# Performance work log

Measured on AMD Instinct MI355X. Metric: run time of the kernel, lower is better.

## Reference

```python
import jax, jax.numpy as jnp
import numpy as np

A = 128       # atom_fea_len
NBR = 41      # nbr_fea_len
H = 128       # h_fea_len_dist == h_fea_len_const
NCONV = 3
EPS = 1e-5    # BatchNorm eps


def leaky(x):
    return jnp.where(x >= 0, x, 0.01 * x)  # LeakyReLU(0.01)


def bn(x2d, g, b):
    # training-mode BatchNorm1d: batch statistics over dim 0 (biased variance)
    mu = x2d.mean(0)
    var = x2d.var(0)
    return g * (x2d - mu) * jax.lax.rsqrt(var + EPS) + b


def setup_inputs() -> dict:
    N, M = 20000, 12
    key = jax.random.key(0)
    ks = jax.random.split(key, 24)
    s = 0.02
    in2 = 2 * A + NBR  # 297
    d = {}
    d["atom_fea"] = jax.random.normal(ks[0], (N, 92), jnp.float32)
    d["nbr_fea"] = jax.random.uniform(ks[1], (N, M, NBR), dtype=jnp.float32)
    d["nbr_fea_offset"] = jax.random.normal(ks[2], (N, M, 3), jnp.float32)
    d["atom_pos"] = jax.random.normal(ks[3], (N, 3), jnp.float32) * 3.0
    d["cells"] = jnp.eye(3, dtype=jnp.float32) * 10.0 + 0.1 * jax.random.normal(ks[4], (3, 3), jnp.float32)
    d["nbr_fea_idx"] = jax.random.randint(ks[5], (N, M), 0, N)
    # embedding
    d["emb_W"] = s * jax.random.normal(ks[6], (A, 92), jnp.float32)
    d["emb_b"] = jnp.zeros((A,), jnp.float32)
    # conv layers (stacked)
    d["convs_W"] = s * jax.random.normal(ks[7], (NCONV, 2 * A, in2), jnp.float32)
    d["convs_b"] = jnp.zeros((NCONV, 2 * A), jnp.float32)
    d["convs_bn1_g"] = jnp.ones((NCONV, 2 * A), jnp.float32)
    d["convs_bn1_b"] = jnp.zeros((NCONV, 2 * A), jnp.float32)
    d["convs_bn2_g"] = jnp.ones((NCONV, A), jnp.float32)
    d["convs_bn2_b"] = jnp.zeros((NCONV, A), jnp.float32)
    # bond_distance head
    d["dist_W"] = s * jax.random.normal(ks[8], (H, in2), jnp.float32)
    d["dist_b"] = jnp.zeros((H,), jnp.float32)
    d["dist_bn_g"] = jnp.ones((H,), jnp.float32)
    d["dist_bn_b"] = jnp.zeros((H,), jnp.float32)
    d["dist2_W"] = s * jax.random.normal(ks[9], (1, H), jnp.float32)
    d["dist2_b"] = jnp.zeros((1,), jnp.float32)
    # bond_constant head
    d["const_W"] = s * jax.random.normal(ks[10], (H, in2), jnp.float32)
    d["const_b"] = jnp.zeros((H,), jnp.float32)
    d["const_bn_g"] = jnp.ones((H,), jnp.float32)
    d["const_bn_b"] = jnp.zeros((H,), jnp.float32)
    d["const2_W"] = s * jax.random.normal(ks[11], (1, H), jnp.float32)
    d["const2_b"] = jnp.zeros((1,), jnp.float32)
    return d


def _forward(atom_fea, nbr_fea, nbr_fea_offset, atom_pos, cells,
             emb_W, emb_b, convs_W, convs_b, convs_bn1_g, convs_bn1_b,
             convs_bn2_g, convs_bn2_b, dist_W, dist_b, dist_bn_g, dist_bn_b,
             dist2_W, dist2_b, const_W, const_b, const_bn_g, const_bn_b,
             const2_W, const2_b, nbr_fea_idx):
    N, M = nbr_fea_idx.shape
    af = atom_fea @ emb_W.T + emb_b  # (N, A) embedding

    # get_distance: PBC distance using fractional offsets and the cell matrix
    nbr_abs = atom_pos[nbr_fea_idx] + jnp.einsum('nmk,kd->nmd', nbr_fea_offset, cells)
    dvec = nbr_abs - atom_pos[:, None, :]
    distance = jnp.sqrt(jnp.sum(dvec * dvec, -1, keepdims=True) + 1e-12)  # (N, M, 1)

    # conv layers: gather -> concat -> linear -> bn -> gate -> sum -> bn -> residual
    for i in range(NCONV):
        total = jnp.concatenate([
            jnp.broadcast_to(af[:, None, :], (N, M, A)),
            af[nbr_fea_idx],
            nbr_fea], axis=2)                                   # (N, M, 2A+NBR)
        g = jnp.einsum('nmf,of->nmo', total, convs_W[i]) + convs_b[i]  # (N, M, 2A)
        g = bn(g.reshape(-1, 2 * A), convs_bn1_g[i], convs_bn1_b[i]).reshape(N, M, 2 * A)
        nbr_filter = jax.nn.sigmoid(g[..., :A])
        nbr_core = leaky(g[..., A:])
        summed = bn((nbr_filter * nbr_core).sum(1), convs_bn2_g[i], convs_bn2_b[i])
        af = leaky(af + summed)

    # bond features
    bond_fea = jnp.concatenate([
        jnp.broadcast_to(af[:, None, :], (N, M, A)),
        af[nbr_fea_idx],
        nbr_fea], axis=2)  # (N, M, 2A+NBR)

    # bond_distance head (LeakyReLU activations)
    bd = jnp.einsum('nmf,hf->nmh', bond_fea, dist_W) + dist_b
    bd = leaky(bn(bd.reshape(-1, H), dist_bn_g, dist_bn_b).reshape(N, M, H))
    bd = leaky(jnp.einsum('nmh,oh->nmo', bd, dist2_W) + dist2_b + distance)  # (N, M, 1)

    # bond_constant head (Softplus activations)
    bc = jnp.einsum('nmf,hf->nmh', bond_fea, const_W) + const_b
    bc = jax.nn.softplus(bn(bc.reshape(-1, H), const_bn_g, const_bn_b).reshape(N, M, H))
    bc = jax.nn.softplus(jnp.einsum('nmh,oh->nmo', bc, const2_W) + const2_b)  # (N, M, 1)

    return jnp.concatenate([bd, bc], axis=-1)  # (N, M, 2)


def reference(atom_fea, nbr_fea, nbr_fea_offset, atom_pos, cells,
              emb_W, emb_b, convs_W, convs_b, convs_bn1_g, convs_bn1_b,
              convs_bn2_g, convs_bn2_b, dist_W, dist_b, dist_bn_g, dist_bn_b,
              dist2_W, dist2_b, const_W, const_b, const_bn_g, const_bn_b,
              const2_W, const2_b, nbr_fea_idx):
    return _forward(atom_fea, nbr_fea, nbr_fea_offset, atom_pos, cells,
                    emb_W, emb_b, convs_W, convs_b, convs_bn1_g, convs_bn1_b,
                    convs_bn2_g, convs_bn2_b, dist_W, dist_b, dist_bn_g, dist_bn_b,
                    dist2_W, dist2_b, const_W, const_b, const_bn_g, const_bn_b,
                    const2_W, const2_b, nbr_fea_idx)
```

## Files before the change

kernel.cpp:

```cpp
#include <hip/hip_runtime.h>
#include <hip/hip_bf16.h>
#include <math.h>

typedef __hip_bfloat16 bf16;

#define AFEA 128
#define NBRF 41
#define IN2 297
#define KP 320
#define TSTR 328
#define ROWS 64
#define P1 64
#define P2 16

typedef __attribute__((ext_vector_type(8))) short bf16x8;
typedef __attribute__((ext_vector_type(4))) float f32x4;

__device__ __forceinline__ unsigned short bfbits(float x) {
    bf16 h = __float2bfloat16(x);
    return *(unsigned short*)&h;
}
__device__ __forceinline__ unsigned int pack2(float x, float y) {
    return (unsigned int)bfbits(x) | ((unsigned int)bfbits(y) << 16);
}
__device__ __forceinline__ float blo(unsigned int u) { return __uint_as_float(u << 16); }
__device__ __forceinline__ float bhi(unsigned int u) { return __uint_as_float(u & 0xffff0000u); }
__device__ __forceinline__ float leakyf(float x) { return x >= 0.f ? x : 0.01f * x; }
__device__ __forceinline__ float sigmoid_fast(float x) { return 1.f / (1.f + __expf(-x)); }
__device__ __forceinline__ float softplus_fast(float x) {
    return fmaxf(x, 0.f) + __logf(1.f + __expf(-fabsf(x)));
}

__global__ void nbr16_kernel(const float* __restrict__ nbr, unsigned short* __restrict__ nbr16,
                             int NM)
{
    int i = blockIdx.x * blockDim.x + threadIdx.x;
    if (i >= NM * 64) return;
    int k = i & 63, e = i >> 6;
    nbr16[i] = (k < NBRF) ? bfbits(nbr[(size_t)e * NBRF + k]) : 0;
}

__global__ __launch_bounds__(256) void embed_kernel(
    const float* __restrict__ xf, const float* __restrict__ W,
    const float* __restrict__ b, float* __restrict__ af,
    unsigned short* __restrict__ af16, int N)
{
    __shared__ float W_s[92 * 128];
    __shared__ float xs[16 * 92];
    int t = threadIdx.x;
    int n0 = blockIdx.x * 16;
    for (int i = t; i < 92 * 128; i += 256) {
        int o = i / 92, k = i - o * 92;
        W_s[k * 128 + o] = W[i];
    }
    for (int i = t; i < 16 * 92; i += 256) {
        int a = i / 92, k = i - a * 92;
        int n = n0 + a;
        xs[i] = (n < N) ? xf[(size_t)n * 92 + k] : 0.f;
    }
    __syncthreads();
    int o = t & 127, h = t >> 7;
    float bias = b[o];
    for (int a = h; a < 16; a += 2) {
        int n = n0 + a;
        if (n >= N) break;
        float acc = bias;
        const float* xr = xs + a * 92;
        #pragma unroll 4
        for (int k = 0; k < 92; k++) acc += xr[k] * W_s[k * 128 + o];
        af[(size_t)n * AFEA + o] = acc;
        af16[(size_t)n * AFEA + o] = bfbits(acc);
    }
}

__global__ void prep_kernel(const float* __restrict__ Wa, size_t offA,
                            const float* __restrict__ Wsrc, size_t offB,
                            unsigned short* __restrict__ Wb,
                            float* __restrict__ zbuf, int nz)
{
    int i = blockIdx.x * blockDim.x + threadIdx.x;
    if (i < nz) zbuf[i] = 0.f;
    if (i >= KP * 256) return;
    int t32 = i & 31;
    int c = (i >> 5) & 255;
    int kc = i >> 13;
    int k = kc * 32 + t32;
    float v = 0.f;
    if (k < IN2) v = (c < 128) ? Wa[offA + (size_t)c * IN2 + k]
                               : Wsrc[offB + (size_t)(c - 128) * IN2 + k];
    Wb[i] = bfbits(v);
}

__global__ __launch_bounds__(256, 3) void gemm_mfma_kernel(
    const unsigned short* __restrict__ af16, const unsigned short* __restrict__ nbr16,
    const int* __restrict__ idx, const unsigned short* __restrict__ Wb,
    const float* __restrict__ bias_a, size_t boffA,
    const float* __restrict__ bias_b, size_t boffB,
    unsigned short* __restrict__ g_t, float* __restrict__ part1,
    int NM, int M)
{
    __shared__ unsigned short a_tile[ROWS * TSTR];
    const int t = threadIdx.x;
    const int e0 = blockIdx.x * ROWS;

    const int l = t & 63, w = t >> 6;
    const int m16 = l & 15, q = l >> 4;
    const int colbase = w * 64;
    const unsigned short* bbase = Wb + (size_t)(colbase + m16) * 32 + q * 8;

    {
        int row = t >> 2, p = t & 3;
        int e = e0 + row;
        int n = e / M;
        int j = idx[e];
        const uint4* srcn = (const uint4*)(af16 + (size_t)n * AFEA);
        const uint4* srcj = (const uint4*)(af16 + (size_t)j * AFEA);
        const uint4* srcb = (const uint4*)(nbr16 + (size_t)e * 64);
        uint4* dst = (uint4*)(a_tile + row * TSTR);
        #pragma unroll
        for (int u = 0; u < 4; u++) dst[p + 4 * u] = srcn[p + 4 * u];
        #pragma unroll
        for (int u = 0; u < 4; u++) dst[16 + p + 4 * u] = srcj[p + 4 * u];
        #pragma unroll
        for (int u = 0; u < 2; u++) dst[32 + p + 4 * u] = srcb[p + 4 * u];
    }

    bf16x8 bcur[4], bnxt[4];
    #pragma unroll
    for (int ct = 0; ct < 4; ct++)
        bcur[ct] = *(const bf16x8*)(bbase + ct * 512);
    #pragma unroll
    for (int ct = 0; ct < 4; ct++)
        bnxt[ct] = *(const bf16x8*)(bbase + 8192 + ct * 512);

    __syncthreads();

    f32x4 acc[4][4];
    #pragma unroll
    for (int rt = 0; rt < 4; rt++)
        #pragma unroll
        for (int ct = 0; ct < 4; ct++) acc[rt][ct] = (f32x4)0.f;

    const unsigned short* abase = a_tile + m16 * TSTR + q * 8;

    #pragma unroll
    for (int kc = 0; kc < KP / 32; kc++) {
        bf16x8 a[4], b2[4];
        if (kc < KP / 32 - 2) {
            #pragma unroll
            for (int ct = 0; ct < 4; ct++)
                b2[ct] = *(const bf16x8*)(bbase + (kc + 2) * 8192 + ct * 512);
        }
        #pragma unroll
        for (int rt = 0; rt < 4; rt++)
            a[rt] = *(const bf16x8*)(abase + rt * 16 * TSTR + kc * 32);
        #pragma unroll
        for (int rt = 0; rt < 4; rt++)
            #pragma unroll
            for (int ct = 0; ct < 4; ct++)
                acc[rt][ct] = __builtin_amdgcn_mfma_f32_16x16x32_bf16(
                    a[rt], bcur[ct], acc[rt][ct], 0, 0, 0);
        if (kc < KP / 32 - 1) {
            #pragma unroll
            for (int ct = 0; ct < 4; ct++) bcur[ct] = bnxt[ct];
        }
        if (kc < KP / 32 - 2) {
            #pragma unroll
            for (int ct = 0; ct < 4; ct++) bnxt[ct] = b2[ct];
        }
    }

    float* pp = part1 + (size_t)(blockIdx.x & (P1 - 1)) * 512;
    #pragma unroll
    for (int ct = 0; ct < 4; ct++) {
        int col = colbase + ct * 16 + m16;
        float bias = (col < 128) ? bias_a[boffA + col] : bias_b[boffB + col - 128];
        float ps = 0.f, pq = 0.f;
        #pragma unroll
        for (int rt = 0; rt < 4; rt++) {
            float v0 = acc[rt][ct][0] + bias;
            float v1 = acc[rt][ct][1] + bias;
            float v2 = acc[rt][ct][2] + bias;
            float v3 = acc[rt][ct][3] + bias;
            ps += (v0 + v1) + (v2 + v3);
            pq += (v0 * v0 + v1 * v1) + (v2 * v2 + v3 * v3);
            uint2 pk;
            pk.x = pack2(v0, v1);
            pk.y = pack2(v2, v3);
            *(uint2*)(g_t + (size_t)col * NM + e0 + rt * 16 + q * 4) = pk;
        }
        ps += __shfl_xor(ps, 16); ps += __shfl_xor(ps, 32);
        pq += __shfl_xor(pq, 16); pq += __shfl_xor(pq, 32);
        if (q == 0) {
            atomicAdd(&pp[col], ps);
            atomicAdd(&pp[256 + col], pq);
        }
    }
}

__global__ __launch_bounds__(256) void gate_kernel(
    const unsigned short* __restrict__ gt, const float* __restrict__ part1,
    const float* __restrict__ gamma, const float* __restrict__ beta,
    float* __restrict__ summed, float* __restrict__ part2,
    float cnt1, int N, int M, int NM)
{
    __shared__ float affA[4 * 16], affC[4 * 16];
    int t = threadIdx.x, w = t >> 6, l = t & 63;
    int cp0 = (blockIdx.x & 3) * 16 + w * 4;
    int fch0 = 2 * cp0;

    if (l < 16) {
        int ch = (l < 8) ? (fch0 + l) : (128 + fch0 + (l - 8));
        float s = 0.f, qq = 0.f;
        #pragma unroll 8
        for (int p = 0; p < P1; p++) {
            s += part1[(size_t)p * 512 + ch];
            qq += part1[(size_t)p * 512 + 256 + ch];
        }
        float mean = s / cnt1;
        float var = fmaxf(qq / cnt1 - mean * mean, 0.f);
        float a = gamma[ch] * rsqrtf(var + 1e-5f);
        affA[w * 16 + l] = a;
        affC[w * 16 + l] = beta[ch] - mean * a;
    }
    __syncthreads();

    int n = (blockIdx.x >> 2) * 64 + l;
    bool act = (n < N);
    size_t col0 = (size_t)n * M;
    float* pp = part2 + (size_t)(blockIdx.x & (P2 - 1)) * 256;
    #pragma unroll
    for (int cpi = 0; cpi < 4; cpi++) {
        int chf = fch0 + 2 * cpi;
        int chc = 128 + chf;
        float s0 = 0.f, s1 = 0.f;
        if (act) {
            const uint2* rf0 = (const uint2*)(gt + (size_t)chf * NM + col0);
            const uint2* rf1 = (const uint2*)(gt + (size_t)(chf + 1) * NM + col0);
            const uint2* rc0 = (const uint2*)(gt + (size_t)chc * NM + col0);
            const uint2* rc1 = (const uint2*)(gt + (size_t)(chc + 1) * NM + col0);
            float aF0 = affA[w * 16 + 2 * cpi],     cF0 = affC[w * 16 + 2 * cpi];
            float aF1 = affA[w * 16 + 2 * cpi + 1], cF1 = affC[w * 16 + 2 * cpi + 1];
            float aC0 = affA[w * 16 + 8 + 2 * cpi],     cC0 = affC[w * 16 + 8 + 2 * cpi];
            float aC1 = affA[w * 16 + 8 + 2 * cpi + 1], cC1 = affC[w * 16 + 8 + 2 * cpi + 1];
            #pragma unroll
            for (int u = 0; u < 3; u++) {
                uint2 f0 = rf0[u], f1 = rf1[u], k0 = rc0[u], k1 = rc1[u];
                #pragma unroll
                for (int h = 0; h < 4; h++) {
                    unsigned int fw0 = (h < 2) ? f0.x : f0.y;
                    unsigned int fw1 = (h < 2) ? f1.x : f1.y;
                    unsigned int kw0 = (h < 2) ? k0.x : k0.y;
                    unsigned int kw1 = (h < 2) ? k1.x : k1.y;
                    float gf0 = (h & 1) ? bhi(fw0) : blo(fw0);
                    float gf1 = (h & 1) ? bhi(fw1) : blo(fw1);
                    float gc0 = (h & 1) ? bhi(kw0) : blo(kw0);
                    float gc1 = (h & 1) ? bhi(kw1) : blo(kw1);
                    s0 += sigmoid_fast(fmaf(aF0, gf0, cF0)) * leakyf(fmaf(aC0, gc0, cC0));
                    s1 += sigmoid_fast(fmaf(aF1, gf1, cF1)) * leakyf(fmaf(aC1, gc1, cC1));
                }
            }
            *(float2*)(summed + (size_t)n * AFEA + chf) = make_float2(s0, s1);
        }
        float q0 = s0 * s0, q1 = s1 * s1;
        #pragma unroll
        for (int sft = 32; sft > 0; sft >>= 1) {
            s0 += __shfl_xor(s0, sft);
            s1 += __shfl_xor(s1, sft);
            q0 += __shfl_xor(q0, sft);
            q1 += __shfl_xor(q1, sft);
        }
        if (l == 0) {
            atomicAdd(&pp[chf], s0);
            atomicAdd(&pp[chf + 1], s1);
            atomicAdd(&pp[128 + chf], q0);
            atomicAdd(&pp[128 + chf + 1], q1);
        }
    }
}

__global__ __launch_bounds__(256) void afup_kernel(
    float* __restrict__ af, unsigned short* __restrict__ af16,
    const float* __restrict__ summed, const float* __restrict__ part2,
    const float* __restrict__ gamma2, const float* __restrict__ beta2,
    float cnt2, int total)
{
    __shared__ float a2s[128], c2s[128];
    int t = threadIdx.x;
    if (t < 128) {
        float s = 0.f, qq = 0.f;
        #pragma unroll
        for (int p = 0; p < P2; p++) {
            s += part2[(size_t)p * 256 + t];
            qq += part2[(size_t)p * 256 + 128 + t];
        }
        float mean = s / cnt2;
        float var = fmaxf(qq / cnt2 - mean * mean, 0.f);
        float a = gamma2[t] * rsqrtf(var + 1e-5f);
        a2s[t] = a;
        c2s[t] = beta2[t] - mean * a;
    }
    __syncthreads();
    int o = t & 127;
    float a2 = a2s[o], c2 = c2s[o];
    int base = blockIdx.x * 2048 + t;
    #pragma unroll
    for (int k = 0; k < 8; k++) {
        int i = base + k * 256;
        if (i < total) {
            float v = af[i] + a2 * summed[i] + c2;
            v = (v >= 0.f) ? v : 0.01f * v;
            af[i] = v;
            af16[i] = bfbits(v);
        }
    }
}

__global__ __launch_bounds__(256) void head_kernel(
    const unsigned short* __restrict__ gt, const float* __restrict__ part1,
    const float* __restrict__ dbg, const float* __restrict__ cbg,
    const float* __restrict__ dbb, const float* __restrict__ cbb,
    const float* __restrict__ w2d, const float* __restrict__ b2d,
    const float* __restrict__ w2c, const float* __restrict__ b2c,
    const float* __restrict__ pos, const float* __restrict__ off,
    const float* __restrict__ cells, const int* __restrict__ idx,
    float* __restrict__ out, float cnt1, int NM, int M)
{
    __shared__ float a_s[256], c_s[256], w_s[256];
    int t = threadIdx.x;
    {
        float s = 0.f, qq = 0.f;
        #pragma unroll 8
        for (int p = 0; p < P1; p++) {
            s += part1[(size_t)p * 512 + t];
            qq += part1[(size_t)p * 512 + 256 + t];
        }
        float mean = s / cnt1;
        float var = fmaxf(qq / cnt1 - mean * mean, 0.f);
        float g  = (t < 128) ? dbg[t] : cbg[t - 128];
        float be = (t < 128) ? dbb[t] : cbb[t - 128];
        float a = g * rsqrtf(var + 1e-5f);
        a_s[t] = a;
        c_s[t] = be - mean * a;
        w_s[t] = (t < 128) ? w2d[t] : w2c[t - 128];
    }
    __syncthreads();

    int e = blockIdx.x * 512 + t * 2;
    if (e >= NM) return;
    float sd0 = 0.f, sd1 = 0.f, sc0 = 0.f, sc1 = 0.f;
    #pragma unroll 4
    for (int ch = 0; ch < 128; ch++) {
        unsigned int u = *(const unsigned int*)(gt + (size_t)ch * NM + e);
        float a = a_s[ch], c = c_s[ch], wv = w_s[ch];
        sd0 += leakyf(fmaf(a, blo(u), c)) * wv;
        sd1 += leakyf(fmaf(a, bhi(u), c)) * wv;
    }
    #pragma unroll 4
    for (int ch = 128; ch < 256; ch++) {
        unsigned int u = *(const unsigned int*)(gt + (size_t)ch * NM + e);
        float a = a_s[ch], c = c_s[ch], wv = w_s[ch];
        sc0 += softplus_fast(fmaf(a, blo(u), c)) * wv;
        sc1 += softplus_fast(fmaf(a, bhi(u), c)) * wv;
    }
    float dist[2];
    #pragma unroll
    for (int h = 0; h < 2; h++) {
        int eb = e + h;
        int n = eb / M;
        int j = idx[eb];
        float o0 = off[(size_t)eb * 3 + 0];
        float o1 = off[(size_t)eb * 3 + 1];
        float o2 = off[(size_t)eb * 3 + 2];
        float d0 = o0 * cells[0] + o1 * cells[3] + o2 * cells[6] + pos[(size_t)j * 3 + 0] - pos[(size_t)n * 3 + 0];
        float d1 = o0 * cells[1] + o1 * cells[4] + o2 * cells[7] + pos[(size_t)j * 3 + 1] - pos[(size_t)n * 3 + 1];
        float d2 = o0 * cells[2] + o1 * cells[5] + o2 * cells[8] + pos[(size_t)j * 3 + 2] - pos[(size_t)n * 3 + 2];
        dist[h] = sqrtf(d0 * d0 + d1 * d1 + d2 * d2 + 1e-12f);
    }
    float bd = b2d[0], bc = b2c[0];
    float4 o4;
    o4.x = leakyf(sd0 + bd + dist[0]);
    o4.y = softplus_fast(sc0 + bc);
    o4.z = leakyf(sd1 + bd + dist[1]);
    o4.w = softplus_fast(sc1 + bc);
    *(float4*)(out + (size_t)e * 2) = o4;
}

extern "C" void kernel_launch(void* const* d_in, const int* in_sizes, int n_in,
                              void* d_out, int out_size, void* d_ws, size_t ws_size,
                              hipStream_t stream) {
    const float* atom_fea   = (const float*)d_in[0];
    const float* nbr_fea    = (const float*)d_in[1];
    const float* nbr_off    = (const float*)d_in[2];
    const float* atom_pos   = (const float*)d_in[3];
    const float* cells      = (const float*)d_in[4];
    const int*   idx        = (const int*)d_in[5];
    const float* emb_W      = (const float*)d_in[6];
    const float* emb_b      = (const float*)d_in[7];
    const float* convs_W    = (const float*)d_in[8];
    const float* convs_b    = (const float*)d_in[9];
    const float* bn1g       = (const float*)d_in[10];
    const float* bn1b       = (const float*)d_in[11];
    const float* bn2g       = (const float*)d_in[12];
    const float* bn2b       = (const float*)d_in[13];
    const float* dist_W     = (const float*)d_in[14];
    const float* dist_b     = (const float*)d_in[15];
    const float* dist_bn_g  = (const float*)d_in[16];
    const float* dist_bn_b  = (const float*)d_in[17];
    const float* dist2_W    = (const float*)d_in[18];
    const float* dist2_b    = (const float*)d_in[19];
    const float* const_W    = (const float*)d_in[20];
    const float* const_b    = (const float*)d_in[21];
    const float* const_bn_g = (const float*)d_in[22];
    const float* const_bn_b = (const float*)d_in[23];
    const float* const2_W   = (const float*)d_in[24];
    const float* const2_b   = (const float*)d_in[25];

    const int N  = in_sizes[0] / 92;
    const int M  = in_sizes[5] / N;
    const int NM = N * M;

    char* ws = (char*)d_ws;
    size_t off = 0;
    float* af             = (float*)(ws + off); off += (size_t)N * AFEA * 4;
    float* summed         = (float*)(ws + off); off += (size_t)N * AFEA * 4;
    unsigned short* af16  = (unsigned short*)(ws + off); off += (size_t)N * AFEA * 2;
    unsigned short* Wb    = (unsigned short*)(ws + off); off += (size_t)256 * KP * 2;
    float* part1          = (float*)(ws + off); off += (size_t)P1 * 512 * 4;
    float* part2          = (float*)(ws + off); off += (size_t)P2 * 256 * 4;
    unsigned short* g_t   = (unsigned short*)(ws + off); off += (size_t)NM * 256 * 2;
    unsigned short* nbr16 = (unsigned short*)(ws + off); off += (size_t)NM * 64 * 2;

    const int NPART = P1 * 512 + P2 * 256;

    nbr16_kernel<<<(NM * 64 + 255) / 256, 256, 0, stream>>>(nbr_fea, nbr16, NM);
    embed_kernel<<<(N + 15) / 16, 256, 0, stream>>>(atom_fea, emb_W, emb_b, af, af16, N);

    const int gblocks = NM / ROWS;
    const int gateblocks = ((N + 63) / 64) * 4;
    const int prepblocks = (256 * KP + 255) / 256;

    for (int i = 0; i < 3; i++) {
        size_t wo  = (size_t)i * 256 * IN2;
        size_t bo  = (size_t)i * 256;
        size_t b2o = (size_t)i * 128;

        prep_kernel<<<prepblocks, 256, 0, stream>>>(
            convs_W, wo, convs_W, wo + (size_t)128 * IN2, Wb, part1, NPART);
        gemm_mfma_kernel<<<gblocks, 256, 0, stream>>>(
            af16, nbr16, idx, Wb, convs_b, bo, convs_b, bo + 128,
            g_t, part1, NM, M);
        gate_kernel<<<gateblocks, 256, 0, stream>>>(
            g_t, part1, bn1g + bo, bn1b + bo, summed, part2, (float)NM, N, M, NM);
        afup_kernel<<<(N * AFEA + 2047) / 2048, 256, 0, stream>>>(
            af, af16, summed, part2, bn2g + b2o, bn2b + b2o, (float)N, N * AFEA);
    }

    {
        prep_kernel<<<prepblocks, 256, 0, stream>>>(
            dist_W, 0, const_W, 0, Wb, part1, P1 * 512);
        gemm_mfma_kernel<<<gblocks, 256, 0, stream>>>(
            af16, nbr16, idx, Wb, dist_b, 0, const_b, 0,
            g_t, part1, NM, M);
        head_kernel<<<(NM + 511) / 512, 256, 0, stream>>>(
            g_t, part1, dist_bn_g, const_bn_g, dist_bn_b, const_bn_b,
            dist2_W, dist2_b, const2_W, const2_b,
            atom_pos, nbr_off, cells, idx, (float*)d_out, (float)NM, NM, M);
    }
}
```

Baseline: 675.5 us.

## Make gather-GEMM persistent with double-buffered async global-to-LDS loads

The gather GEMM becomes a persistent kernel with a grid of at most 512 blocks, each looping over 64-row tiles. The next tile's gathered rows (atom, neighbour atom, bond features) are prefetched into a second LDS buffer with global_load_lds direct-to-LDS loads while the current tile is computed. The LDS layout changes to a k-chunk-major arrangement, and weights are kept in a 4-deep register ring. This is meant to hide gather latency and launch overhead, at the cost of doubled LDS use, lower occupancy (launch bounds go from 3 to 2 blocks per unit), and reliance on the async LDS loads being ordered by the barrier.

```diff
diff --git a/kernel.cpp b/kernel.cpp
--- a/kernel.cpp
+++ b/kernel.cpp
@@ -8,8 +8,8 @@
 #define NBRF 41
 #define IN2 297
 #define KP 320
-#define TSTR 328
 #define ROWS 64
+#define GBLK 512
 #define P1 64
 #define P2 16
 
@@ -29,6 +29,14 @@
 __device__ __forceinline__ float sigmoid_fast(float x) { return 1.f / (1.f + __expf(-x)); }
 __device__ __forceinline__ float softplus_fast(float x) {
     return fmaxf(x, 0.f) + __logf(1.f + __expf(-fabsf(x)));
+}
+
+__device__ __forceinline__ void gload16(const unsigned short* g, unsigned short* lds) {
+    auto g1 = (const __attribute__((address_space(1))) void*)(
+        reinterpret_cast<uintptr_t>(g));
+    auto l3 = (__attribute__((address_space(3))) void*)(
+        (unsigned int)(reinterpret_cast<uintptr_t>(lds)));
+    __builtin_amdgcn_global_load_lds(g1, l3, 16, 0, 0);
 }
 
 __global__ void nbr16_kernel(const float* __restrict__ nbr, unsigned short* __restrict__ nbr16,
@@ -91,110 +99,136 @@
     Wb[i] = bfbits(v);
 }
 
-__global__ __launch_bounds__(256, 3) void gemm_mfma_kernel(
+__global__ __launch_bounds__(256, 2) void gemm_mfma_kernel(
     const unsigned short* __restrict__ af16, const unsigned short* __restrict__ nbr16,
     const int* __restrict__ idx, const unsigned short* __restrict__ Wb,
     const float* __restrict__ bias_a, size_t boffA,
     const float* __restrict__ bias_b, size_t boffB,
     unsigned short* __restrict__ g_t, float* __restrict__ part1,
-    int NM, int M)
-{
-    __shared__ unsigned short a_tile[ROWS * TSTR];
+    int NM, int M, int ntiles)
+{
+    __shared__ unsigned short a_tile[2][40 * 512];
+
     const int t = threadIdx.x;
-    const int e0 = blockIdx.x * ROWS;
-
     const int l = t & 63, w = t >> 6;
     const int m16 = l & 15, q = l >> 4;
     const int colbase = w * 64;
     const unsigned short* bbase = Wb + (size_t)(colbase + m16) * 32 + q * 8;
 
-    {
-        int row = t >> 2, p = t & 3;
-        int e = e0 + row;
-        int n = e / M;
-        int j = idx[e];
-        const uint4* srcn = (const uint4*)(af16 + (size_t)n * AFEA);
-        const uint4* srcj = (const uint4*)(af16 + (size_t)j * AFEA);
-        const uint4* srcb = (const uint4*)(nbr16 + (size_t)e * 64);
-        uint4* dst = (uint4*)(a_tile + row * TSTR);
-        #pragma unroll
-        for (int u = 0; u < 4; u++) dst[p + 4 * u] = srcn[p + 4 * u];
-        #pragma unroll
-        for (int u = 0; u < 4; u++) dst[16 + p + 4 * u] = srcj[p + 4 * u];
-        #pragma unroll
-        for (int u = 0; u < 2; u++) dst[32 + p + 4 * u] = srcb[p + 4 * u];
-    }
-
-    bf16x8 bcur[4], bnxt[4];
+    int tile = blockIdx.x;
+
+    bf16x8 bb[4][4];
     #pragma unroll
-    for (int ct = 0; ct < 4; ct++)
-        bcur[ct] = *(const bf16x8*)(bbase + ct * 512);
-    #pragma unroll
-    for (int ct = 0; ct < 4; ct++)
-        bnxt[ct] = *(const bf16x8*)(bbase + 8192 + ct * 512);
-
+    for (int c = 0; c < 4; c++)
+        #pragma unroll
+        for (int ct = 0; ct < 4; ct++)
+            bb[c][ct] = *(const bf16x8*)(bbase + c * 8192 + ct * 512);
+
+    int jreg = 0;
+    if (tile < ntiles) {
+        int e = tile * ROWS + l;
+        int j0 = idx[e];
+        int n0 = e / M;
+        unsigned short* bp = a_tile[0];
+        const unsigned short* srcn = af16 + (size_t)n0 * AFEA;
+        const unsigned short* srcj = af16 + (size_t)j0 * AFEA;
+        const unsigned short* srcb = nbr16 + (size_t)e * 64;
+        #pragma unroll
+        for (int i = 0; i < 4; i++) gload16(srcn + (4 * w + i) * 8, bp + (4 * w + i) * 512);
+        #pragma unroll
+        for (int i = 0; i < 4; i++) gload16(srcj + (4 * w + i) * 8, bp + (16 + 4 * w + i) * 512);
+        #pragma unroll
+        for (int i = 0; i < 2; i++) gload16(srcb + (2 * w + i) * 8, bp + (32 + 2 * w + i) * 512);
+        int e1 = (tile + GBLK) * ROWS + l;
+        jreg = idx[e1 < NM ? e1 : 0];
+    }
     __syncthreads();
 
-    f32x4 acc[4][4];
-    #pragma unroll
-    for (int rt = 0; rt < 4; rt++)
-        #pragma unroll
-        for (int ct = 0; ct < 4; ct++) acc[rt][ct] = (f32x4)0.f;
-
-    const unsigned short* abase = a_tile + m16 * TSTR + q * 8;
-
-    #pragma unroll
-    for (int kc = 0; kc < KP / 32; kc++) {
-        bf16x8 a[4], b2[4];
-        if (kc < KP / 32 - 2) {
-            #pragma unroll
-            for (int ct = 0; ct < 4; ct++)
-                b2[ct] = *(const bf16x8*)(bbase + (kc + 2) * 8192 + ct * 512);
-        }
+    int it = 0;
+    for (; tile < ntiles; tile += GBLK, it ^= 1) {
+        const int e0 = tile * ROWS;
+        unsigned short* bufc = a_tile[it];
+        unsigned short* bufn = a_tile[it ^ 1];
+
+        if (tile + GBLK < ntiles) {
+            int en = (tile + GBLK) * ROWS + l;
+            int nn = en / M;
+            const unsigned short* srcn = af16 + (size_t)nn * AFEA;
+            const unsigned short* srcj = af16 + (size_t)jreg * AFEA;
+            const unsigned short* srcb = nbr16 + (size_t)en * 64;
+            #pragma unroll
+            for (int i = 0; i < 4; i++) gload16(srcn + (4 * w + i) * 8, bufn + (4 * w + i) * 512);
+            #pragma unroll
+            for (int i = 0; i < 4; i++) gload16(srcj + (4 * w + i) * 8, bufn + (16 + 4 * w + i) * 512);
+            #pragma unroll
+            for (int i = 0; i < 2; i++) gload16(srcb + (2 * w + i) * 8, bufn + (32 + 2 * w + i) * 512);
+            int e2 = en + GBLK * ROWS;
+            jreg = idx[e2 < NM ? e2 : 0];
+        }
+
+        f32x4 acc[4][4];
         #pragma unroll
         for (int rt = 0; rt < 4; rt++)
-            a[rt] = *(const bf16x8*)(abase + rt * 16 * TSTR + kc * 32);
-        #pragma unroll
-        for (int rt = 0; rt < 4; rt++)
-            #pragma unroll
-            for (int ct = 0; ct < 4; ct++)
-                acc[rt][ct] = __builtin_amdgcn_mfma_f32_16x16x32_bf16(
-                    a[rt], bcur[ct], acc[rt][ct], 0, 0, 0);
-        if (kc < KP / 32 - 1) {
-            #pragma unroll
-            for (int ct = 0; ct < 4; ct++) bcur[ct] = bnxt[ct];
-        }
-        if (kc < KP / 32 - 2) {
-            #pragma unroll
-            for (int ct = 0; ct < 4; ct++) bnxt[ct] = b2[ct];
-        }
-    }
-
-    float* pp = part1 + (size_t)(blockIdx.x & (P1 - 1)) * 512;
-    #pragma unroll
-    for (int ct = 0; ct < 4; ct++) {
-        int col = colbase + ct * 16 + m16;
-        float bias = (col < 128) ? bias_a[boffA + col] : bias_b[boffB + col - 128];
-        float ps = 0.f, pq = 0.f;
-        #pragma unroll
-        for (int rt = 0; rt < 4; rt++) {
-            float v0 = acc[rt][ct][0] + bias;
-            float v1 = acc[rt][ct][1] + bias;
-            float v2 = acc[rt][ct][2] + bias;
-            float v3 = acc[rt][ct][3] + bias;
-            ps += (v0 + v1) + (v2 + v3);
-            pq += (v0 * v0 + v1 * v1) + (v2 * v2 + v3 * v3);
-            uint2 pk;
-            pk.x = pack2(v0, v1);
-            pk.y = pack2(v2, v3);
-            *(uint2*)(g_t + (size_t)col * NM + e0 + rt * 16 + q * 4) = pk;
-        }
-        ps += __shfl_xor(ps, 16); ps += __shfl_xor(ps, 32);
-        pq += __shfl_xor(pq, 16); pq += __shfl_xor(pq, 32);
-        if (q == 0) {
-            atomicAdd(&pp[col], ps);
-            atomicAdd(&pp[256 + col], pq);
-        }
+            #pragma unroll
+            for (int ct = 0; ct < 4; ct++) acc[rt][ct] = (f32x4)0.f;
+
+        const unsigned short* abase = bufc + q * 512 + m16 * 8;
+
+        #pragma unroll
+        for (int kc = 0; kc < KP / 32; kc++) {
+            bf16x8 a[4];
+            #pragma unroll
+            for (int rt = 0; rt < 4; rt++)
+                a[rt] = *(const bf16x8*)(abase + kc * 2048 + rt * 128);
+            #pragma unroll
+            for (int rt = 0; rt < 4; rt++)
+                #pragma unroll
+                for (int ct = 0; ct < 4; ct++)
+                    acc[rt][ct] = __builtin_amdgcn_mfma_f32_16x16x32_bf16(
+                        a[rt], bb[kc & 3][ct], acc[rt][ct], 0, 0, 0);
+            if (kc < 6) {
+                #pragma unroll
+                for (int ct = 0; ct < 4; ct++)
+                    bb[kc & 3][ct] = *(const bf16x8*)(bbase + (kc + 4) * 8192 + ct * 512);
+            }
+        }
+
+        if (tile + GBLK < ntiles) {
+            #pragma unroll
+            for (int c = 0; c < 4; c++)
+                #pragma unroll
+                for (int ct = 0; ct < 4; ct++)
+                    bb[c][ct] = *(const bf16x8*)(bbase + c * 8192 + ct * 512);
+        }
+
+        float* pp = part1 + (size_t)(blockIdx.x & (P1 - 1)) * 512;
+        #pragma unroll
+        for (int ct = 0; ct < 4; ct++) {
+            int col = colbase + ct * 16 + m16;
+            float bias = (col < 128) ? bias_a[boffA + col] : bias_b[boffB + col - 128];
+            float ps = 0.f, pq = 0.f;
+            #pragma unroll
+            for (int rt = 0; rt < 4; rt++) {
+                float v0 = acc[rt][ct][0] + bias;
+                float v1 = acc[rt][ct][1] + bias;
+                float v2 = acc[rt][ct][2] + bias;
+                float v3 = acc[rt][ct][3] + bias;
+                ps += (v0 + v1) + (v2 + v3);
+                pq += (v0 * v0 + v1 * v1) + (v2 * v2 + v3 * v3);
+                uint2 pk;
+                pk.x = pack2(v0, v1);
+                pk.y = pack2(v2, v3);
+                *(uint2*)(g_t + (size_t)col * NM + e0 + rt * 16 + q * 4) = pk;
+            }
+            ps += __shfl_xor(ps, 16); ps += __shfl_xor(ps, 32);
+            pq += __shfl_xor(pq, 16); pq += __shfl_xor(pq, 32);
+            if (q == 0) {
+                atomicAdd(&pp[col], ps);
+                atomicAdd(&pp[256 + col], pq);
+            }
+        }
+
+        __syncthreads();
     }
 }
 
@@ -437,6 +471,7 @@
     embed_kernel<<<(N + 15) / 16, 256, 0, stream>>>(atom_fea, emb_W, emb_b, af, af16, N);
 
     const int gblocks = NM / ROWS;
+    const int ggrid = gblocks < GBLK ? gblocks : GBLK;
     const int gateblocks = ((N + 63) / 64) * 4;
     const int prepblocks = (256 * KP + 255) / 256;
 
@@ -447,9 +482,9 @@
 
         prep_kernel<<<prepblocks, 256, 0, stream>>>(
             convs_W, wo, convs_W, wo + (size_t)128 * IN2, Wb, part1, NPART);
-        gemm_mfma_kernel<<<gblocks, 256, 0, stream>>>(
+        gemm_mfma_kernel<<<ggrid, 256, 0, stream>>>(
             af16, nbr16, idx, Wb, convs_b, bo, convs_b, bo + 128,
-            g_t, part1, NM, M);
+            g_t, part1, NM, M, gblocks);
         gate_kernel<<<gateblocks, 256, 0, stream>>>(
             g_t, part1, bn1g + bo, bn1b + bo, summed, part2, (float)NM, N, M, NM);
         afup_kernel<<<(N * AFEA + 2047) / 2048, 256, 0, stream>>>(
@@ -459,9 +494,9 @@
     {
         prep_kernel<<<prepblocks, 256, 0, stream>>>(
             dist_W, 0, const_W, 0, Wb, part1, P1 * 512);
-        gemm_mfma_kernel<<<gblocks, 256, 0, stream>>>(
+        gemm_mfma_kernel<<<ggrid, 256, 0, stream>>>(
             af16, nbr16, idx, Wb, dist_b, 0, const_b, 0,
-            g_t, part1, NM, M);
+            g_t, part1, NM, M, gblocks);
         head_kernel<<<(NM + 511) / 512, 256, 0, stream>>>(
             g_t, part1, dist_bn_g, const_bn_g, dist_bn_b, const_bn_b,
             dist2_W, dist2_b, const2_W, const2_b,
```

New measurement: 806.9 us. +19.5%, slower.

## Recompute conv GEMM in two passes instead of storing gated activations

Applied to the files above, without the earlier changes.

Each conv layer now runs the gather-GEMM twice. The first pass only accumulates BatchNorm statistics. The second recomputes the GEMM and applies BN, sigmoid·leaky gating and the neighbour sum in the epilogue through LDS, with atomics into the summed buffer. This removes the write and reread of the large channel-major g_t intermediate, at the cost of doubling MFMA and gather work. Weight preparation for all four GEMMs is also hoisted into one kernel, using a channel permutation so filter and core channels land in the same wave. A separate sumstats kernel and bn1fin kernel are added, and zeroing moves into other kernels.

```diff
diff --git a/kernel.cpp b/kernel.cpp
--- a/kernel.cpp
+++ b/kernel.cpp
@@ -12,6 +12,7 @@
 #define ROWS 64
 #define P1 64
 #define P2 16
+#define LSP 130
 
 typedef __attribute__((ext_vector_type(8))) short bf16x8;
 typedef __attribute__((ext_vector_type(4))) float f32x4;
@@ -29,6 +30,12 @@
 __device__ __forceinline__ float sigmoid_fast(float x) { return 1.f / (1.f + __expf(-x)); }
 __device__ __forceinline__ float softplus_fast(float x) {
     return fmaxf(x, 0.f) + __logf(1.f + __expf(-fabsf(x)));
+}
+
+__device__ __forceinline__ int permch(int slot) {
+    int w = slot >> 6, ct = (slot >> 4) & 3, m = slot & 15;
+    int base = w * 32 + (ct & 1) * 16 + m;
+    return (ct < 2) ? base : 128 + base;
 }
 
 __global__ void nbr16_kernel(const float* __restrict__ nbr, unsigned short* __restrict__ nbr16,
@@ -73,40 +80,38 @@
     }
 }
 
-__global__ void prep_kernel(const float* __restrict__ Wa, size_t offA,
-                            const float* __restrict__ Wsrc, size_t offB,
-                            unsigned short* __restrict__ Wb,
-                            float* __restrict__ zbuf, int nz)
+__global__ void prep_all_kernel(const float* __restrict__ convs_W,
+                                const float* __restrict__ dist_W,
+                                const float* __restrict__ const_W,
+                                unsigned short* __restrict__ Wb4,
+                                float* __restrict__ zbuf, int nz)
 {
     int i = blockIdx.x * blockDim.x + threadIdx.x;
     if (i < nz) zbuf[i] = 0.f;
-    if (i >= KP * 256) return;
-    int t32 = i & 31;
-    int c = (i >> 5) & 255;
-    int kc = i >> 13;
+    if (i >= 4 * KP * 256) return;
+    int s = i / (KP * 256);
+    int r = i - s * (KP * 256);
+    int t32 = r & 31;
+    int c = (r >> 5) & 255;
+    int kc = r >> 13;
     int k = kc * 32 + t32;
     float v = 0.f;
-    if (k < IN2) v = (c < 128) ? Wa[offA + (size_t)c * IN2 + k]
-                               : Wsrc[offB + (size_t)(c - 128) * IN2 + k];
-    Wb[i] = bfbits(v);
-}
-
-__global__ __launch_bounds__(256, 3) void gemm_mfma_kernel(
+    if (k < IN2) {
+        if (s < 3) v = convs_W[((size_t)s * 256 + permch(c)) * IN2 + k];
+        else       v = (c < 128) ? dist_W[(size_t)c * IN2 + k]
+                                 : const_W[(size_t)(c - 128) * IN2 + k];
+    }
+    Wb4[i] = bfbits(v);
+}
+
+__device__ __forceinline__ void gemm_core(
     const unsigned short* __restrict__ af16, const unsigned short* __restrict__ nbr16,
     const int* __restrict__ idx, const unsigned short* __restrict__ Wb,
-    const float* __restrict__ bias_a, size_t boffA,
-    const float* __restrict__ bias_b, size_t boffB,
-    unsigned short* __restrict__ g_t, float* __restrict__ part1,
-    int NM, int M)
-{
-    __shared__ unsigned short a_tile[ROWS * TSTR];
-    const int t = threadIdx.x;
-    const int e0 = blockIdx.x * ROWS;
-
+    unsigned short* a_tile, int e0, int M, int t, f32x4 (&acc)[4][4])
+{
     const int l = t & 63, w = t >> 6;
     const int m16 = l & 15, q = l >> 4;
-    const int colbase = w * 64;
-    const unsigned short* bbase = Wb + (size_t)(colbase + m16) * 32 + q * 8;
+    const unsigned short* bbase = Wb + (size_t)(w * 64 + m16) * 32 + q * 8;
 
     {
         int row = t >> 2, p = t & 3;
@@ -135,7 +140,6 @@
 
     __syncthreads();
 
-    f32x4 acc[4][4];
     #pragma unroll
     for (int rt = 0; rt < 4; rt++)
         #pragma unroll
@@ -169,12 +173,197 @@
             for (int ct = 0; ct < 4; ct++) bnxt[ct] = b2[ct];
         }
     }
-
+}
+
+__global__ __launch_bounds__(256, 3) void gemm_stats_kernel(
+    const unsigned short* __restrict__ af16, const unsigned short* __restrict__ nbr16,
+    const int* __restrict__ idx, const unsigned short* __restrict__ Wb,
+    const float* __restrict__ bias256, float* __restrict__ part1,
+    float* __restrict__ summed, int NM, int M, int nsum)
+{
+    __shared__ __align__(16) unsigned short a_tile[ROWS * TSTR];
+    int t = threadIdx.x;
+    for (int i = blockIdx.x * 256 + t; i < nsum; i += gridDim.x * 256) summed[i] = 0.f;
+
+    f32x4 acc[4][4];
+    gemm_core(af16, nbr16, idx, Wb, a_tile, blockIdx.x * ROWS, M, t, acc);
+
+    const int l = t & 63, w = t >> 6, m16 = l & 15, q = l >> 4;
     float* pp = part1 + (size_t)(blockIdx.x & (P1 - 1)) * 512;
     #pragma unroll
     for (int ct = 0; ct < 4; ct++) {
-        int col = colbase + ct * 16 + m16;
-        float bias = (col < 128) ? bias_a[boffA + col] : bias_b[boffB + col - 128];
+        int col = w * 64 + ct * 16 + m16;
+        float bias = bias256[permch(col)];
+        float ps = 0.f, pq = 0.f;
+        #pragma unroll
+        for (int rt = 0; rt < 4; rt++) {
+            float v0 = acc[rt][ct][0] + bias;
+            float v1 = acc[rt][ct][1] + bias;
+            float v2 = acc[rt][ct][2] + bias;
+            float v3 = acc[rt][ct][3] + bias;
+            ps += (v0 + v1) + (v2 + v3);
+            pq += (v0 * v0 + v1 * v1) + (v2 * v2 + v3 * v3);
+        }
+        ps += __shfl_xor(ps, 16); ps += __shfl_xor(ps, 32);
+        pq += __shfl_xor(pq, 16); pq += __shfl_xor(pq, 32);
+        if (q == 0) {
+            atomicAdd(&pp[col], ps);
+            atomicAdd(&pp[256 + col], pq);
+        }
+    }
+}
+
+__global__ __launch_bounds__(256) void bn1fin_kernel(
+    const float* __restrict__ part1, const float* __restrict__ gamma,
+    const float* __restrict__ beta, float* __restrict__ aff,
+    float* __restrict__ part2, float cnt1)
+{
+    int t = threadIdx.x;
+    #pragma unroll
+    for (int k = 0; k < P2; k++) part2[k * 256 + t] = 0.f;
+    float s = 0.f, qq = 0.f;
+    #pragma unroll 8
+    for (int p = 0; p < P1; p++) {
+        s  += part1[(size_t)p * 512 + t];
+        qq += part1[(size_t)p * 512 + 256 + t];
+    }
+    float mean = s / cnt1;
+    float var = fmaxf(qq / cnt1 - mean * mean, 0.f);
+    int ch = permch(t);
+    float a = gamma[ch] * rsqrtf(var + 1e-5f);
+    aff[t] = a;
+    aff[256 + t] = beta[ch] - mean * a;
+}
+
+__global__ __launch_bounds__(256, 3) void gemm_gate_kernel(
+    const unsigned short* __restrict__ af16, const unsigned short* __restrict__ nbr16,
+    const int* __restrict__ idx, const unsigned short* __restrict__ Wb,
+    const float* __restrict__ bias256, const float* __restrict__ aff,
+    float* __restrict__ summed, int NM, int M)
+{
+    __shared__ __align__(16) unsigned short a_tile[ROWS * TSTR];
+    float* ls = (float*)a_tile;
+    int t = threadIdx.x;
+    const int e0 = blockIdx.x * ROWS;
+
+    f32x4 acc[4][4];
+    gemm_core(af16, nbr16, idx, Wb, a_tile, e0, M, t, acc);
+
+    const int l = t & 63, w = t >> 6, m16 = l & 15, q = l >> 4;
+
+    __syncthreads();
+
+    #pragma unroll
+    for (int ct = 0; ct < 2; ct++) {
+        int sf  = w * 64 + ct * 16 + m16;
+        int fch = w * 32 + ct * 16 + m16;
+        float aF = aff[sf],      cF = aff[256 + sf];
+        float aC = aff[sf + 32], cC = aff[256 + sf + 32];
+        cF = fmaf(aF, bias256[fch], cF);
+        cC = fmaf(aC, bias256[128 + fch], cC);
+        #pragma unroll
+        for (int rt = 0; rt < 4; rt++) {
+            int rbase = rt * 16 + q * 4;
+            #pragma unroll
+            for (int j = 0; j < 4; j++) {
+                float zf = fmaf(aF, acc[rt][ct][j], cF);
+                float zc = fmaf(aC, acc[rt][ct + 2][j], cC);
+                ls[(rbase + j) * LSP + fch] = sigmoid_fast(zf) * leakyf(zc);
+            }
+        }
+    }
+    __syncthreads();
+
+    int nfirst = e0 / M;
+    int nlast  = (e0 + ROWS - 1) / M;
+    int ntasks = (nlast - nfirst + 1) * 128;
+    for (int task = t; task < ntasks; task += 256) {
+        int ai = task >> 7, c = task & 127;
+        int n = nfirst + ai;
+        int lo = n * M - e0;           if (lo < 0) lo = 0;
+        int hi = n * M + M - 1 - e0;   if (hi > ROWS - 1) hi = ROWS - 1;
+        float s = 0.f;
+        for (int r = lo; r <= hi; r++) s += ls[r * LSP + c];
+        atomicAdd(&summed[(size_t)n * AFEA + c], s);
+    }
+}
+
+__global__ __launch_bounds__(256) void sumstats_kernel(
+    const float* __restrict__ summed, float* __restrict__ part2, int N)
+{
+    int t = threadIdx.x;
+    int c = t & 127, h = t >> 7;
+    int n0 = blockIdx.x * 128;
+    float s = 0.f, qq = 0.f;
+    for (int a = h; a < 128; a += 2) {
+        int n = n0 + a;
+        if (n >= N) break;
+        float v = summed[(size_t)n * AFEA + c];
+        s += v; qq += v * v;
+    }
+    float* pp = part2 + (size_t)(blockIdx.x & (P2 - 1)) * 256;
+    atomicAdd(&pp[c], s);
+    atomicAdd(&pp[128 + c], qq);
+}
+
+__global__ __launch_bounds__(256) void afup_kernel(
+    float* __restrict__ af, unsigned short* __restrict__ af16,
+    const float* __restrict__ summed, const float* __restrict__ part2,
+    const float* __restrict__ gamma2, const float* __restrict__ beta2,
+    float* __restrict__ part1, float cnt2, int total)
+{
+    __shared__ float a2s[128], c2s[128];
+    int t = threadIdx.x;
+    if (blockIdx.x < 128) part1[blockIdx.x * 256 + t] = 0.f;
+    if (t < 128) {
+        float s = 0.f, qq = 0.f;
+        #pragma unroll
+        for (int p = 0; p < P2; p++) {
+            s += part2[(size_t)p * 256 + t];
+            qq += part2[(size_t)p * 256 + 128 + t];
+        }
+        float mean = s / cnt2;
+        float var = fmaxf(qq / cnt2 - mean * mean, 0.f);
+        float a = gamma2[t] * rsqrtf(var + 1e-5f);
+        a2s[t] = a;
+        c2s[t] = beta2[t] - mean * a;
+    }
+    __syncthreads();
+    int o = t & 127;
+    float a2 = a2s[o], c2 = c2s[o];
+    int base = blockIdx.x * 2048 + t;
+    #pragma unroll
+    for (int k = 0; k < 8; k++) {
+        int i = base + k * 256;
+        if (i < total) {
+            float v = af[i] + a2 * summed[i] + c2;
+            v = (v >= 0.f) ? v : 0.01f * v;
+            af[i] = v;
+            af16[i] = bfbits(v);
+        }
+    }
+}
+
+__global__ __launch_bounds__(256, 3) void gemm_mfma_kernel(
+    const unsigned short* __restrict__ af16, const unsigned short* __restrict__ nbr16,
+    const int* __restrict__ idx, const unsigned short* __restrict__ Wb,
+    const float* __restrict__ bias_a, const float* __restrict__ bias_b,
+    unsigned short* __restrict__ g_t, float* __restrict__ part1,
+    int NM, int M)
+{
+    __shared__ __align__(16) unsigned short a_tile[ROWS * TSTR];
+    int t = threadIdx.x;
+    const int e0 = blockIdx.x * ROWS;
+
+    f32x4 acc[4][4];
+    gemm_core(af16, nbr16, idx, Wb, a_tile, e0, M, t, acc);
+
+    const int l = t & 63, w = t >> 6, m16 = l & 15, q = l >> 4;
+    float* pp = part1 + (size_t)(blockIdx.x & (P1 - 1)) * 512;
+    #pragma unroll
+    for (int ct = 0; ct < 4; ct++) {
+        int col = w * 64 + ct * 16 + m16;
+        float bias = (col < 128) ? bias_a[col] : bias_b[col - 128];
         float ps = 0.f, pq = 0.f;
         #pragma unroll
         for (int rt = 0; rt < 4; rt++) {
@@ -194,124 +383,6 @@
         if (q == 0) {
             atomicAdd(&pp[col], ps);
             atomicAdd(&pp[256 + col], pq);
-        }
-    }
-}
-
-__global__ __launch_bounds__(256) void gate_kernel(
-    const unsigned short* __restrict__ gt, const float* __restrict__ part1,
-    const float* __restrict__ gamma, const float* __restrict__ beta,
-    float* __restrict__ summed, float* __restrict__ part2,
-    float cnt1, int N, int M, int NM)
-{
-    __shared__ float affA[4 * 16], affC[4 * 16];
-    int t = threadIdx.x, w = t >> 6, l = t & 63;
-    int cp0 = (blockIdx.x & 3) * 16 + w * 4;
-    int fch0 = 2 * cp0;
-
-    if (l < 16) {
-        int ch = (l < 8) ? (fch0 + l) : (128 + fch0 + (l - 8));
-        float s = 0.f, qq = 0.f;
-        #pragma unroll 8
-        for (int p = 0; p < P1; p++) {
-            s += part1[(size_t)p * 512 + ch];
-            qq += part1[(size_t)p * 512 + 256 + ch];
-        }
-        float mean = s / cnt1;
-        float var = fmaxf(qq / cnt1 - mean * mean, 0.f);
-        float a = gamma[ch] * rsqrtf(var + 1e-5f);
-        affA[w * 16 + l] = a;
-        affC[w * 16 + l] = beta[ch] - mean * a;
-    }
-    __syncthreads();
-
-    int n = (blockIdx.x >> 2) * 64 + l;
-    bool act = (n < N);
-    size_t col0 = (size_t)n * M;
-    float* pp = part2 + (size_t)(blockIdx.x & (P2 - 1)) * 256;
-    #pragma unroll
-    for (int cpi = 0; cpi < 4; cpi++) {
-        int chf = fch0 + 2 * cpi;
-        int chc = 128 + chf;
-        float s0 = 0.f, s1 = 0.f;
-        if (act) {
-            const uint2* rf0 = (const uint2*)(gt + (size_t)chf * NM + col0);
-            const uint2* rf1 = (const uint2*)(gt + (size_t)(chf + 1) * NM + col0);
-            const uint2* rc0 = (const uint2*)(gt + (size_t)chc * NM + col0);
-            const uint2* rc1 = (const uint2*)(gt + (size_t)(chc + 1) * NM + col0);
-            float aF0 = affA[w * 16 + 2 * cpi],     cF0 = affC[w * 16 + 2 * cpi];
-            float aF1 = affA[w * 16 + 2 * cpi + 1], cF1 = affC[w * 16 + 2 * cpi + 1];
-            float aC0 = affA[w * 16 + 8 + 2 * cpi],     cC0 = affC[w * 16 + 8 + 2 * cpi];
-            float aC1 = affA[w * 16 + 8 + 2 * cpi + 1], cC1 = affC[w * 16 + 8 + 2 * cpi + 1];
-            #pragma unroll
-            for (int u = 0; u < 3; u++) {
-                uint2 f0 = rf0[u], f1 = rf1[u], k0 = rc0[u], k1 = rc1[u];
-                #pragma unroll
-                for (int h = 0; h < 4; h++) {
-                    unsigned int fw0 = (h < 2) ? f0.x : f0.y;
-                    unsigned int fw1 = (h < 2) ? f1.x : f1.y;
-                    unsigned int kw0 = (h < 2) ? k0.x : k0.y;
-                    unsigned int kw1 = (h < 2) ? k1.x : k1.y;
-                    float gf0 = (h & 1) ? bhi(fw0) : blo(fw0);
-                    float gf1 = (h & 1) ? bhi(fw1) : blo(fw1);
-                    float gc0 = (h & 1) ? bhi(kw0) : blo(kw0);
-                    float gc1 = (h & 1) ? bhi(kw1) : blo(kw1);
-                    s0 += sigmoid_fast(fmaf(aF0, gf0, cF0)) * leakyf(fmaf(aC0, gc0, cC0));
-                    s1 += sigmoid_fast(fmaf(aF1, gf1, cF1)) * leakyf(fmaf(aC1, gc1, cC1));
-                }
-            }
-            *(float2*)(summed + (size_t)n * AFEA + chf) = make_float2(s0, s1);
-        }
-        float q0 = s0 * s0, q1 = s1 * s1;
-        #pragma unroll
-        for (int sft = 32; sft > 0; sft >>= 1) {
-            s0 += __shfl_xor(s0, sft);
-            s1 += __shfl_xor(s1, sft);
-            q0 += __shfl_xor(q0, sft);
-            q1 += __shfl_xor(q1, sft);
-        }
-        if (l == 0) {
-            atomicAdd(&pp[chf], s0);
-            atomicAdd(&pp[chf + 1], s1);
-            atomicAdd(&pp[128 + chf], q0);
-            atomicAdd(&pp[128 + chf + 1], q1);
-        }
-    }
-}
-
-__global__ __launch_bounds__(256) void afup_kernel(
-    float* __restrict__ af, unsigned short* __restrict__ af16,
-    const float* __restrict__ summed, const float* __restrict__ part2,
-    const float* __restrict__ gamma2, const float* __restrict__ beta2,
-    float cnt2, int total)
-{
-    __shared__ float a2s[128], c2s[128];
-    int t = threadIdx.x;
-    if (t < 128) {
-        float s = 0.f, qq = 0.f;
-        #pragma unroll
-        for (int p = 0; p < P2; p++) {
-            s += part2[(size_t)p * 256 + t];
-            qq += part2[(size_t)p * 256 + 128 + t];
-        }
-        float mean = s / cnt2;
-        float var = fmaxf(qq / cnt2 - mean * mean, 0.f);
-        float a = gamma2[t] * rsqrtf(var + 1e-5f);
-        a2s[t] = a;
-        c2s[t] = beta2[t] - mean * a;
-    }
-    __syncthreads();
-    int o = t & 127;
-    float a2 = a2s[o], c2 = c2s[o];
-    int base = blockIdx.x * 2048 + t;
-    #pragma unroll
-    for (int k = 0; k < 8; k++) {
-        int i = base + k * 256;
-        if (i < total) {
-            float v = af[i] + a2 * summed[i] + c2;
-            v = (v >= 0.f) ? v : 0.01f * v;
-            af[i] = v;
-            af16[i] = bfbits(v);
         }
     }
 }
@@ -425,42 +496,41 @@
     float* af             = (float*)(ws + off); off += (size_t)N * AFEA * 4;
     float* summed         = (float*)(ws + off); off += (size_t)N * AFEA * 4;
     unsigned short* af16  = (unsigned short*)(ws + off); off += (size_t)N * AFEA * 2;
-    unsigned short* Wb    = (unsigned short*)(ws + off); off += (size_t)256 * KP * 2;
+    unsigned short* Wb4   = (unsigned short*)(ws + off); off += (size_t)4 * 256 * KP * 2;
     float* part1          = (float*)(ws + off); off += (size_t)P1 * 512 * 4;
     float* part2          = (float*)(ws + off); off += (size_t)P2 * 256 * 4;
+    float* aff            = (float*)(ws + off); off += (size_t)512 * 4;
     unsigned short* g_t   = (unsigned short*)(ws + off); off += (size_t)NM * 256 * 2;
     unsigned short* nbr16 = (unsigned short*)(ws + off); off += (size_t)NM * 64 * 2;
 
     const int NPART = P1 * 512 + P2 * 256;
 
+    prep_all_kernel<<<(4 * KP * 256 + 255) / 256, 256, 0, stream>>>(
+        convs_W, dist_W, const_W, Wb4, part1, NPART);
     nbr16_kernel<<<(NM * 64 + 255) / 256, 256, 0, stream>>>(nbr_fea, nbr16, NM);
     embed_kernel<<<(N + 15) / 16, 256, 0, stream>>>(atom_fea, emb_W, emb_b, af, af16, N);
 
     const int gblocks = NM / ROWS;
-    const int gateblocks = ((N + 63) / 64) * 4;
-    const int prepblocks = (256 * KP + 255) / 256;
+    const int ssblocks = (N + 127) / 128;
 
     for (int i = 0; i < 3; i++) {
-        size_t wo  = (size_t)i * 256 * IN2;
-        size_t bo  = (size_t)i * 256;
-        size_t b2o = (size_t)i * 128;
-
-        prep_kernel<<<prepblocks, 256, 0, stream>>>(
-            convs_W, wo, convs_W, wo + (size_t)128 * IN2, Wb, part1, NPART);
+        const unsigned short* Wbi = Wb4 + (size_t)i * KP * 256;
+        const float* cb  = convs_b + (size_t)i * 256;
+        gemm_stats_kernel<<<gblocks, 256, 0, stream>>>(
+            af16, nbr16, idx, Wbi, cb, part1, summed, NM, M, N * AFEA);
+        bn1fin_kernel<<<1, 256, 0, stream>>>(
+            part1, bn1g + (size_t)i * 256, bn1b + (size_t)i * 256, aff, part2, (float)NM);
+        gemm_gate_kernel<<<gblocks, 256, 0, stream>>>(
+            af16, nbr16, idx, Wbi, cb, aff, summed, NM, M);
+        sumstats_kernel<<<ssblocks, 256, 0, stream>>>(summed, part2, N);
+        afup_kernel<<<(N * AFEA + 2047) / 2048, 256, 0, stream>>>(
+            af, af16, summed, part2, bn2g + (size_t)i * 128, bn2b + (size_t)i * 128,
+            part1, (float)N, N * AFEA);
+    }
+
+    {
         gemm_mfma_kernel<<<gblocks, 256, 0, stream>>>(
-            af16, nbr16, idx, Wb, convs_b, bo, convs_b, bo + 128,
-            g_t, part1, NM, M);
-        gate_kernel<<<gateblocks, 256, 0, stream>>>(
-            g_t, part1, bn1g + bo, bn1b + bo, summed, part2, (float)NM, N, M, NM);
-        afup_kernel<<<(N * AFEA + 2047) / 2048, 256, 0, stream>>>(
-            af, af16, summed, part2, bn2g + b2o, bn2b + b2o, (float)N, N * AFEA);
-    }
-
-    {
-        prep_kernel<<<prepblocks, 256, 0, stream>>>(
-            dist_W, 0, const_W, 0, Wb, part1, P1 * 512);
-        gemm_mfma_kernel<<<gblocks, 256, 0, stream>>>(
-            af16, nbr16, idx, Wb, dist_b, 0, const_b, 0,
+            af16, nbr16, idx, Wb4 + (size_t)3 * KP * 256, dist_b, const_b,
             g_t, part1, NM, M);
         head_kernel<<<(NM + 511) / 512, 256, 0, stream>>>(
             g_t, part1, dist_bn_g, const_bn_g, dist_bn_b, const_bn_b,
```

After: 749.7 us. +11.0%, slower.
